# Kernel optimization log

Hardware: AMD Instinct MI355X
Metric: run time of the kernel (lower is better)

## Reference

```python
import jax, jax.numpy as jnp
import numpy as np

N = 16384   # total gate nodes (64 graphs x 256 gates)
B = 64      # graphs in batch
E = 49152   # directed edges (avg in-degree 3)
Q = 32      # qubit_num
F = 256     # feat_dim
D = 2 * F   # node feature dim = 512
H = 2       # heads
A = 128     # action_num


def _gatv2(x, wl, wr, att, b, src, dst, n):
    # PyG GATv2Conv (concat=True, share_weights=False, negative_slope=0.2)
    h, c = att.shape
    xl = (x @ wl).reshape(n, h, c)   # source-side projection [N,H,C]
    xr = (x @ wr).reshape(n, h, c)   # target-side projection [N,H,C]
    e = jax.nn.leaky_relu(xl[src] + xr[dst], 0.2)       # [E,H,C]
    logit = jnp.einsum('ehc,hc->eh', e, att)             # [E,H]
    m = jax.ops.segment_max(logit, dst, num_segments=n)  # softmax over in-edges per target
    p = jnp.exp(logit - m[dst])
    den = jax.ops.segment_sum(p, dst, num_segments=n)
    alpha = p / den[dst]                                 # [E,H]
    out = jax.ops.segment_sum(alpha[:, :, None] * xl[src], dst, num_segments=n)
    return out.reshape(n, h * c) + b


def _forward(x, xt_w1, xt_b1, xt_w2, xt_b2,
             g0_wl, g0_wr, g0_att, g0_b,
             g1_wl, g1_wr, g1_att, g1_b,
             g2_wl, g2_wr, g2_att, g2_b,
             g3_wl, g3_wr, g3_att, g3_b,
             g4_wl, g4_wr, g4_att, g4_b,
             ln_w, ln_b, aggr_t,
             m_w1, m_b1, m_w2, m_b2, m_w3, m_b3,
             edge_index, batch):
    lr = lambda v: jax.nn.leaky_relu(v, 0.01)
    # x_trans: Linear -> LeakyReLU -> Linear, then fold qubit-pairs into one node
    h0 = lr(x @ xt_w1 + xt_b1) @ xt_w2 + xt_b2           # [2N, F]
    cx = h0.reshape(-1, D)                               # [N, 2F]
    n = cx.shape[0]
    # GATv2Conv default add_self_loops=True (inputs contain no self loops)
    sl = jnp.arange(n, dtype=edge_index.dtype)
    src = jnp.concatenate([edge_index[0], sl])
    dst = jnp.concatenate([edge_index[1], sl])
    res = cx
    h = lr(_gatv2(cx, g0_wl, g0_wr, g0_att, g0_b, src, dst, n))
    for wl_, wr_, att_, b_ in ((g1_wl, g1_wr, g1_att, g1_b),
                               (g2_wl, g2_wr, g2_att, g2_b),
                               (g3_wl, g3_wr, g3_att, g3_b)):
        h = lr(_gatv2(h, wl_, wr_, att_, b_, src, dst, n))
    h = lr(_gatv2(h, g4_wl, g4_wr, g4_att, g4_b, src, dst, n))
    h = h + res                                           # residual [N, 2F]
    # PyG LayerNorm(mode='graph'): normalize over nodes AND channels per graph
    cnt = jax.ops.segment_sum(jnp.ones((n,), h.dtype), batch, num_segments=B)
    norm = cnt * h.shape[1]
    mean = jax.ops.segment_sum(h.sum(-1), batch, num_segments=B) / norm
    hc = h - mean[batch][:, None]
    var = jax.ops.segment_sum((hc * hc).sum(-1), batch, num_segments=B) / norm
    h = hc / jnp.sqrt(var + 1e-5)[batch][:, None] * ln_w + ln_b
    # SoftmaxAggregation(learn=True): channel-wise softmax over nodes per graph
    logit = h * aggr_t
    mg = jax.ops.segment_max(logit, batch, num_segments=B)
    p = jnp.exp(logit - mg[batch])
    den = jax.ops.segment_sum(p, batch, num_segments=B)
    g = jax.ops.segment_sum((p / den[batch]) * h, batch, num_segments=B)  # [B, 2F]
    # head MLP 512->384->256->128
    o = lr(g @ m_w1 + m_b1)
    o = lr(o @ m_w2 + m_b2)
    return o @ m_w3 + m_b3


def setup_inputs() -> dict:
    key = jax.random.key(0)
    ks = iter(jax.random.split(key, 64))
    def rn(shp, s=0.05):
        return jax.random.normal(next(ks), shp, jnp.float32) * s
    d = {}
    d['x'] = jax.random.normal(next(ks), (2 * N, Q), jnp.float32)
    src = jax.random.randint(next(ks), (E,), 0, N, jnp.int32)
    off = jax.random.randint(next(ks), (E,), 1, N, jnp.int32)
    d['edge_index'] = jnp.stack([src, (src + off) % N])  # no self loops
    d['batch'] = jnp.arange(N, dtype=jnp.int32) // (N // B)
    d['xt_w1'] = rn((Q, F)); d['xt_b1'] = rn((F,))
    d['xt_w2'] = rn((F, F)); d['xt_b2'] = rn((F,))
    d['g0_wl'] = rn((D, H * D)); d['g0_wr'] = rn((D, H * D))
    d['g0_att'] = rn((H, D));    d['g0_b'] = rn((H * D,))
    for i in (1, 2, 3):
        d[f'g{i}_wl'] = rn((H * D, H * D)); d[f'g{i}_wr'] = rn((H * D, H * D))
        d[f'g{i}_att'] = rn((H, D));        d[f'g{i}_b'] = rn((H * D,))
    d['g4_wl'] = rn((H * D, D)); d['g4_wr'] = rn((H * D, D))
    d['g4_att'] = rn((1, D));    d['g4_b'] = rn((D,))
    d['ln_w'] = jnp.ones((D,), jnp.float32); d['ln_b'] = jnp.zeros((D,), jnp.float32)
    d['aggr_t'] = jnp.array(1.0, jnp.float32)
    d['m_w1'] = rn((D, 384)); d['m_b1'] = rn((384,))
    d['m_w2'] = rn((384, 256)); d['m_b2'] = rn((256,))
    d['m_w3'] = rn((256, A)); d['m_b3'] = rn((A,))
    return d


def reference(x, edge_index, batch, xt_w1, xt_b1, xt_w2, xt_b2,
              g0_wl, g0_wr, g0_att, g0_b,
              g1_wl, g1_wr, g1_att, g1_b,
              g2_wl, g2_wr, g2_att, g2_b,
              g3_wl, g3_wr, g3_att, g3_b,
              g4_wl, g4_wr, g4_att, g4_b,
              ln_w, ln_b, aggr_t,
              m_w1, m_b1, m_w2, m_b2, m_w3, m_b3):
    return _forward(x, xt_w1, xt_b1, xt_w2, xt_b2,
                    g0_wl, g0_wr, g0_att, g0_b,
                    g1_wl, g1_wr, g1_att, g1_b,
                    g2_wl, g2_wr, g2_att, g2_b,
                    g3_wl, g3_wr, g3_att, g3_b,
                    g4_wl, g4_wr, g4_att, g4_b,
                    ln_w, ln_b, aggr_t,
                    m_w1, m_b1, m_w2, m_b2, m_w3, m_b3,
                    edge_index, batch)
```

## Files before the change

kernel.cpp:

```cpp
#include <hip/hip_runtime.h>
#include <hip/hip_bf16.h>

typedef __hip_bfloat16 bf16;

#define NN 16384
#define BBG 64
#define EE 49152
#define ET (EE + NN)
#define DD 512
#define NG (NN / BBG)

__device__ __forceinline__ float b2f(bf16 v) { return __bfloat162float(v); }
__device__ __forceinline__ bf16 f2b(float v) { return __float2bfloat16(v); }
__device__ __forceinline__ float sb2f(short s) {
    unsigned u = ((unsigned)(unsigned short)s) << 16;
    return __builtin_bit_cast(float, u);
}
__device__ __forceinline__ short f2bs(float v) {
    bf16 b = f2b(v);
    return __builtin_bit_cast(short, b);
}
__device__ __forceinline__ int clampi(int v, int lo, int hi)
{
    return v < lo ? lo : (v > hi ? hi : v);
}

typedef __attribute__((ext_vector_type(8))) short bf16x8;
typedef __attribute__((ext_vector_type(4))) float f32x4;

#define AS1 __attribute__((address_space(1)))
#define AS3 __attribute__((address_space(3)))

__global__ __launch_bounds__(256) void gemm_mfma_bt(
    const bf16* __restrict__ A, const bf16* __restrict__ Bt,
    const float* __restrict__ bias, float* __restrict__ C,
    bf16* __restrict__ Cb, int M, int N, int K, float slope, int has_act)
{
    __shared__ bf16 As[128 * 32];
    __shared__ bf16 Bs[128 * 32];
    const int tid = threadIdx.x;
    const int w = tid >> 6;
    const int l = tid & 63;
    const int bm = blockIdx.y * 128;
    const int bn = blockIdx.x * 128;
    const int wrow = (w >> 1) * 64;
    const int wcol = (w & 1) * 64;
    const int quad = l >> 4;
    const int c16 = l & 15;

    const int lrow = l >> 2;
    const int lchunk = l & 3;
    const bf16* Ag = A + (size_t)(bm + w * 16 + lrow) * K + lchunk * 8;
    const bf16* Bg = Bt + (size_t)(bn + w * 16 + lrow) * K + lchunk * 8;
    char* AsB = (char*)As;
    char* BsB = (char*)Bs;

    f32x4 acc[4][4] = {};

    for (int k0 = 0; k0 < K; k0 += 32) {
        __builtin_amdgcn_global_load_lds((const AS1 void*)(Ag + k0),
            (AS3 void*)(AsB + w * 1024), 16, 0, 0);
        __builtin_amdgcn_global_load_lds((const AS1 void*)(Ag + (size_t)64 * K + k0),
            (AS3 void*)(AsB + 4096 + w * 1024), 16, 0, 0);
        __builtin_amdgcn_global_load_lds((const AS1 void*)(Bg + k0),
            (AS3 void*)(BsB + w * 1024), 16, 0, 0);
        __builtin_amdgcn_global_load_lds((const AS1 void*)(Bg + (size_t)64 * K + k0),
            (AS3 void*)(BsB + 4096 + w * 1024), 16, 0, 0);
        __syncthreads();

        bf16x8 a[4], b[4];
#pragma unroll
        for (int i = 0; i < 4; i++) {
            int ra = wrow + i * 16 + c16;
            a[i] = *(const bf16x8*)(AsB + ra * 64 + quad * 16);
            int rb = wcol + i * 16 + c16;
            b[i] = *(const bf16x8*)(BsB + rb * 64 + quad * 16);
        }
#pragma unroll
        for (int i = 0; i < 4; i++)
#pragma unroll
            for (int j = 0; j < 4; j++)
                acc[i][j] = __builtin_amdgcn_mfma_f32_16x16x32_bf16(
                    a[i], b[j], acc[i][j], 0, 0, 0);
        __syncthreads();
    }

#pragma unroll
    for (int i = 0; i < 4; i++) {
#pragma unroll
        for (int j = 0; j < 4; j++) {
            int col = bn + wcol + j * 16 + c16;
            float bv = bias ? bias[col] : 0.f;
#pragma unroll
            for (int r = 0; r < 4; r++) {
                int row = bm + wrow + i * 16 + quad * 4 + r;
                float v = acc[i][j][r] + bv;
                if (has_act) v = (v >= 0.f) ? v : v * slope;
                if (C)  C[(size_t)row * N + col] = v;
                if (Cb) Cb[(size_t)row * N + col] = f2b(v);
            }
        }
    }
}

__global__ __launch_bounds__(256) void gemm_mfma_dual(
    const bf16* __restrict__ A, const bf16* __restrict__ Bt,
    bf16* __restrict__ X0, bf16* __restrict__ X1,
    int M, int Ntot, int K, int HC)
{
    __shared__ bf16 As[128 * 32];
    __shared__ bf16 Bs[128 * 32];
    const int tid = threadIdx.x;
    const int w = tid >> 6;
    const int l = tid & 63;
    const int bm = blockIdx.y * 128;
    const int bn = blockIdx.x * 128;
    const int wrow = (w >> 1) * 64;
    const int wcol = (w & 1) * 64;
    const int quad = l >> 4;
    const int c16 = l & 15;

    const int lrow = l >> 2;
    const int lchunk = l & 3;
    const bf16* Ag = A + (size_t)(bm + w * 16 + lrow) * K + lchunk * 8;
    const bf16* Bg = Bt + (size_t)(bn + w * 16 + lrow) * K + lchunk * 8;
    char* AsB = (char*)As;
    char* BsB = (char*)Bs;

    f32x4 acc[4][4] = {};

    for (int k0 = 0; k0 < K; k0 += 32) {
        __builtin_amdgcn_global_load_lds((const AS1 void*)(Ag + k0),
            (AS3 void*)(AsB + w * 1024), 16, 0, 0);
        __builtin_amdgcn_global_load_lds((const AS1 void*)(Ag + (size_t)64 * K + k0),
            (AS3 void*)(AsB + 4096 + w * 1024), 16, 0, 0);
        __builtin_amdgcn_global_load_lds((const AS1 void*)(Bg + k0),
            (AS3 void*)(BsB + w * 1024), 16, 0, 0);
        __builtin_amdgcn_global_load_lds((const AS1 void*)(Bg + (size_t)64 * K + k0),
            (AS3 void*)(BsB + 4096 + w * 1024), 16, 0, 0);
        __syncthreads();

        bf16x8 a[4], b[4];
#pragma unroll
        for (int i = 0; i < 4; i++) {
            int ra = wrow + i * 16 + c16;
            a[i] = *(const bf16x8*)(AsB + ra * 64 + quad * 16);
            int rb = wcol + i * 16 + c16;
            b[i] = *(const bf16x8*)(BsB + rb * 64 + quad * 16);
        }
#pragma unroll
        for (int i = 0; i < 4; i++)
#pragma unroll
            for (int j = 0; j < 4; j++)
                acc[i][j] = __builtin_amdgcn_mfma_f32_16x16x32_bf16(
                    a[i], b[j], acc[i][j], 0, 0, 0);
        __syncthreads();
    }

#pragma unroll
    for (int i = 0; i < 4; i++) {
#pragma unroll
        for (int j = 0; j < 4; j++) {
            int col = bn + wcol + j * 16 + c16;
            bf16* dst = (col < HC) ? (X0 + col) : (X1 + col - HC);
#pragma unroll
            for (int r = 0; r < 4; r++) {
                int row = bm + wrow + i * 16 + quad * 4 + r;
                dst[(size_t)row * HC] = f2b(acc[i][j][r]);
            }
        }
    }
}

__global__ __launch_bounds__(256) void gemm_f32(
    const float* __restrict__ A, const float* __restrict__ W,
    const float* __restrict__ bias, float* __restrict__ C,
    int M, int N, int K, float slope, int has_act)
{
    const int BK = 16;
    __shared__ float Asm[BK][64 + 1];
    __shared__ float Wsm[BK][64 + 1];
    int tid = threadIdx.x;
    int bm = blockIdx.y * 64;
    int bn = blockIdx.x * 64;
    int tr = tid >> 4;
    int tc = tid & 15;
    float acc[4][4] = {};

    for (int k0 = 0; k0 < K; k0 += BK) {
        {
            int col = tid & 15;
            int row = tid >> 4;
#pragma unroll
            for (int p = 0; p < 4; p++) {
                int r = row + p * 16;
                Asm[col][r] = A[(size_t)(bm + r) * K + k0 + col];
            }
        }
        {
            int wc = tid & 63;
            int wr = tid >> 6;
#pragma unroll
            for (int p = 0; p < 4; p++) {
                int r = wr + p * 4;
                Wsm[r][wc] = W[(size_t)(k0 + r) * N + bn + wc];
            }
        }
        __syncthreads();
#pragma unroll
        for (int kk = 0; kk < BK; kk++) {
            float a[4], w[4];
#pragma unroll
            for (int i = 0; i < 4; i++) a[i] = Asm[kk][tr * 4 + i];
#pragma unroll
            for (int j = 0; j < 4; j++) w[j] = Wsm[kk][tc * 4 + j];
#pragma unroll
            for (int i = 0; i < 4; i++)
#pragma unroll
                for (int j = 0; j < 4; j++)
                    acc[i][j] += a[i] * w[j];
        }
        __syncthreads();
    }
#pragma unroll
    for (int i = 0; i < 4; i++) {
        int r = bm + tr * 4 + i;
#pragma unroll
        for (int j = 0; j < 4; j++) {
            int cn = bn + tc * 4 + j;
            float v = acc[i][j];
            if (bias) v += bias[cn];
            if (has_act) v = (v >= 0.f) ? v : v * slope;
            C[(size_t)r * N + cn] = v;
        }
    }
}

__global__ __launch_bounds__(256) void transpose_f2b2(
    const float* __restrict__ in0, bf16* __restrict__ out0,
    const float* __restrict__ in1, bf16* __restrict__ out1, int R, int C)
{
    const float* in = blockIdx.z ? in1 : in0;
    bf16* out = blockIdx.z ? out1 : out0;
    __shared__ float tile[32][33];
    int c0 = blockIdx.x * 32;
    int r0 = blockIdx.y * 32;
    int tx = threadIdx.x & 31;
    int ty = threadIdx.x >> 5;
#pragma unroll
    for (int k = 0; k < 4; k++) {
        int r = ty + k * 8;
        tile[r][tx] = in[(size_t)(r0 + r) * C + c0 + tx];
    }
    __syncthreads();
#pragma unroll
    for (int k = 0; k < 4; k++) {
        int rr = ty + k * 8;
        out[(size_t)(c0 + rr) * R + r0 + tx] = f2b(tile[tx][rr]);
    }
}

__global__ void f2b_vec(const float* __restrict__ in, bf16* __restrict__ out, int n)
{
    int i = blockIdx.x * 256 + threadIdx.x;
    if (i < n) out[i] = f2b(in[i]);
}

__global__ void count_deg(const int* __restrict__ ei, int* __restrict__ deg)
{
    int e = blockIdx.x * 256 + threadIdx.x;
    if (e >= ET) return;
    int d = (e < EE) ? ei[EE + e] : (e - EE);
    d = clampi(d, 0, NN - 1);
    atomicAdd(&deg[d], 1);
}

__global__ __launch_bounds__(256) void scan_deg(const int* __restrict__ deg,
                                                int* __restrict__ rs)
{
    __shared__ int part[256];
    __shared__ int psum[257];
    int tid = threadIdx.x;
    const int per = NN / 256;
    int base = tid * per;
    int s = 0;
    for (int i = 0; i < per; i++) s += deg[base + i];
    part[tid] = s;
    __syncthreads();
    if (tid == 0) {
        int acc = 0;
        for (int i = 0; i < 256; i++) { psum[i] = acc; acc += part[i]; }
        psum[256] = acc;
    }
    __syncthreads();
    int acc = psum[tid];
    for (int i = 0; i < per; i++) { rs[base + i] = acc; acc += deg[base + i]; }
    if (tid == 0) rs[NN] = psum[256];
}

__global__ void fill_csr(const int* __restrict__ ei, const int* __restrict__ rs,
                         int* __restrict__ cur, int* __restrict__ csrc)
{
    int e = blockIdx.x * 256 + threadIdx.x;
    if (e >= ET) return;
    int s, d;
    if (e < EE) { s = ei[e]; d = ei[EE + e]; } else { s = d = e - EE; }
    s = clampi(s, 0, NN - 1);
    d = clampi(d, 0, NN - 1);
    int pos = atomicAdd(&cur[d], 1);
    int slot = clampi(rs[d] + pos, 0, ET - 1);
    csrc[slot] = s;
}

template<int HC, int PF>
__global__ __launch_bounds__(256, 4) void gat_wave3(
    const bf16* __restrict__ xl, const bf16* __restrict__ xr,
    const float* __restrict__ att, const float* __restrict__ bias,
    const int* __restrict__ rs, const int* __restrict__ csrc,
    const float* __restrict__ res, float* __restrict__ out_f,
    bf16* __restrict__ out_b, float* __restrict__ lnsums)
{
    constexpr int CPL = HC / 64;
    constexpr int NV = CPL / 8;
    const int tid = threadIdx.x;
    const int w = tid >> 6;
    const int lane = tid & 63;
    const int n = blockIdx.x * 4 + w;
    const int c0 = lane * CPL;

    int start = rs[n];
    int deg = clampi(rs[n + 1] - start, 1, 64);
    start = clampi(start, 0, ET - 1);
    start = __builtin_amdgcn_readfirstlane(start);
    deg = __builtin_amdgcn_readfirstlane(deg);
    int my_src = 0;
    if (lane < deg) my_src = clampi(csrc[start + lane], 0, NN - 1);

    bf16x8 rp[NV];
#pragma unroll
    for (int v = 0; v < NV; v++)
        rp[v] = *(const bf16x8*)(xr + (size_t)n * HC + c0 + v * 8);
    float av[CPL];
#pragma unroll
    for (int k = 0; k < CPL; k++) av[k] = att[c0 + k];

    bf16x8 rows[PF][NV];
#pragma unroll
    for (int r = 0; r < PF; r++) {
        if (r < deg) {
            int s = __shfl(my_src, r);
            const bf16* rpp = xl + (size_t)s * HC + c0;
#pragma unroll
            for (int v = 0; v < NV; v++) rows[r][v] = *(const bf16x8*)(rpp + v * 8);
        }
    }
    __builtin_amdgcn_sched_barrier(0);

    float rv[CPL];
#pragma unroll
    for (int k = 0; k < CPL; k++) rv[k] = sb2f(rp[k / 8][k % 8]);

    float part[PF];
#pragma unroll
    for (int r = 0; r < PF; r++) part[r] = -1e30f;
#pragma unroll
    for (int r = 0; r < PF; r++) {
        if (r < deg) {
            float p0 = 0.f, p1 = 0.f, p2 = 0.f, p3 = 0.f;
#pragma unroll
            for (int k = 0; k < CPL; k += 4) {
                float x0 = sb2f(rows[r][(k + 0) / 8][(k + 0) % 8]);
                float x1 = sb2f(rows[r][(k + 1) / 8][(k + 1) % 8]);
                float x2 = sb2f(rows[r][(k + 2) / 8][(k + 2) % 8]);
                float x3 = sb2f(rows[r][(k + 3) / 8][(k + 3) % 8]);
                float u0 = x0 + rv[k + 0]; u0 = (u0 >= 0.f) ? u0 : 0.2f * u0;
                float u1 = x1 + rv[k + 1]; u1 = (u1 >= 0.f) ? u1 : 0.2f * u1;
                float u2 = x2 + rv[k + 2]; u2 = (u2 >= 0.f) ? u2 : 0.2f * u2;
                float u3 = x3 + rv[k + 3]; u3 = (u3 >= 0.f) ? u3 : 0.2f * u3;
                p0 = fmaf(av[k + 0], u0, p0);
                p1 = fmaf(av[k + 1], u1, p1);
                p2 = fmaf(av[k + 2], u2, p2);
                p3 = fmaf(av[k + 3], u3, p3);
            }
            part[r] = (p0 + p1) + (p2 + p3);
        }
    }

    constexpr int MSK0 = (HC == 1024) ? 16 : 32;
#pragma unroll
    for (int msk = MSK0; msk; msk >>= 1) {
#pragma unroll
        for (int r = 0; r < PF; r++)
            if (r < deg) part[r] += __shfl_xor(part[r], msk);
    }

    float m = part[0];
#pragma unroll
    for (int r = 1; r < PF; r++)
        if (r < deg) m = fmaxf(m, part[r]);
    float den = 0.f;
    float pw[PF];
#pragma unroll
    for (int r = 0; r < PF; r++) {
        pw[r] = 0.f;
        if (r < deg) { pw[r] = __expf(part[r] - m); den += pw[r]; }
    }

    float acc[CPL];
#pragma unroll
    for (int k = 0; k < CPL; k++) acc[k] = 0.f;
#pragma unroll
    for (int r = 0; r < PF; r++) {
        if (r < deg) {
#pragma unroll
            for (int k = 0; k < CPL; k++)
                acc[k] = fmaf(pw[r], sb2f(rows[r][k / 8][k % 8]), acc[k]);
        }
    }

    if (deg > PF) {
        auto process = [&](bf16x8 (&rw)[NV]) {
            float part_t = 0.f;
#pragma unroll
            for (int k = 0; k < CPL; k++) {
                float x = sb2f(rw[k / 8][k % 8]);
                float u = x + rv[k];
                u = (u >= 0.f) ? u : 0.2f * u;
                part_t = fmaf(av[k], u, part_t);
            }
#pragma unroll
            for (int msk = MSK0; msk; msk >>= 1) part_t += __shfl_xor(part_t, msk);
            float lg = part_t;
            float mn = fmaxf(m, lg);
            float rr = __expf(m - mn);
            float pi = __expf(lg - mn);
            m = mn;
            den = den * rr + pi;
#pragma unroll
            for (int k = 0; k < CPL; k++) {
                float x = sb2f(rw[k / 8][k % 8]);
                acc[k] = fmaf(acc[k], rr, pi * x);
            }
        };
        bf16x8 curv[NV], nxt[NV];
        {
            int s = __shfl(my_src, PF);
            const bf16* rpp = xl + (size_t)s * HC + c0;
#pragma unroll
            for (int v = 0; v < NV; v++) curv[v] = *(const bf16x8*)(rpp + v * 8);
        }
        for (int i = PF; i < deg; i++) {
            if (i + 1 < deg) {
                int s = __shfl(my_src, i + 1);
                const bf16* rpp = xl + (size_t)s * HC + c0;
#pragma unroll
                for (int v = 0; v < NV; v++) nxt[v] = *(const bf16x8*)(rpp + v * 8);
            }
            process(curv);
#pragma unroll
            for (int v = 0; v < NV; v++) curv[v] = nxt[v];
        }
    }

    float inv = 1.f / den;
    float ls = 0.f, ls2 = 0.f;
    float vals[CPL];
#pragma unroll
    for (int k = 0; k < CPL; k++) {
        float v = fmaf(acc[k], inv, bias[c0 + k]);
        v = (v >= 0.f) ? v : 0.01f * v;
        vals[k] = v;
    }
    if (res) {
#pragma unroll
        for (int k = 0; k < CPL; k++) {
            vals[k] += res[(size_t)n * HC + c0 + k];
            ls += vals[k];
            ls2 += vals[k] * vals[k];
        }
#pragma unroll
        for (int v = 0; v < NV * 2; v++) {
            f32x4 ov;
#pragma unroll
            for (int k = 0; k < 4; k++) ov[k] = vals[v * 4 + k];
            *(f32x4*)(out_f + (size_t)n * HC + c0 + v * 4) = ov;
        }
    } else {
#pragma unroll
        for (int v = 0; v < NV; v++) {
            bf16x8 ov;
#pragma unroll
            for (int k = 0; k < 8; k++) ov[k] = f2bs(vals[v * 8 + k]);
            *(bf16x8*)(out_b + (size_t)n * HC + c0 + v * 8) = ov;
        }
    }

    if (lnsums) {
#pragma unroll
        for (int msk = 32; msk; msk >>= 1) {
            ls += __shfl_xor(ls, msk);
            ls2 += __shfl_xor(ls2, msk);
        }
        if (lane == 0) {
            int g = n >> 8;
            atomicAdd(&lnsums[g], ls);
            atomicAdd(&lnsums[BBG + g], ls2);
        }
    }
}

__global__ __launch_bounds__(256) void aggr_partial(
    const float* __restrict__ h, const float* __restrict__ lnsums,
    const float* __restrict__ lnw, const float* __restrict__ lnb,
    const float* __restrict__ t_, float* __restrict__ pm,
    float* __restrict__ pd, float* __restrict__ pa)
{
    int g = blockIdx.x, ch = blockIdx.y, nk = blockIdx.z;
    int tid = threadIdx.x;
    int c = ch * 256 + tid;
    const float tot = (float)(NG * DD);
    float S = lnsums[g], S2 = lnsums[BBG + g];
    float mu = S / tot;
    float iv = rsqrtf(fmaxf(S2 / tot - mu * mu, 0.f) + 1e-5f);
    float w = lnw[c], b = lnb[c], t = t_[0];
    size_t base = (size_t)g * NG * DD + (size_t)nk * 32 * DD + c;
    float m = -1e30f, den = 0.f, acc = 0.f;
    for (int i = 0; i < 32; i++) {
        float hn = (h[base + (size_t)i * DD] - mu) * iv * w + b;
        float lg = hn * t;
        if (lg > m) {
            float r = __expf(m - lg);
            den *= r; acc *= r; m = lg;
        }
        float p = __expf(lg - m);
        den += p; acc += p * hn;
    }
    size_t idx = (((size_t)g * 2 + ch) * 8 + nk) * 256 + tid;
    pm[idx] = m; pd[idx] = den; pa[idx] = acc;
}

__global__ __launch_bounds__(256) void aggr_combine(
    const float* __restrict__ pm, const float* __restrict__ pd,
    const float* __restrict__ pa, float* __restrict__ gout)
{
    int g = blockIdx.x, ch = blockIdx.y;
    int tid = threadIdx.x;
    size_t base = (((size_t)g * 2 + ch) * 8) * 256 + tid;
    float m = -1e30f;
#pragma unroll
    for (int k = 0; k < 8; k++) m = fmaxf(m, pm[base + k * 256]);
    float den = 0.f, acc = 0.f;
#pragma unroll
    for (int k = 0; k < 8; k++) {
        float r = __expf(pm[base + k * 256] - m);
        den += pd[base + k * 256] * r;
        acc += pa[base + k * 256] * r;
    }
    gout[(size_t)g * DD + ch * 256 + tid] = acc / den;
}

extern "C" void kernel_launch(void* const* d_in, const int* in_sizes, int n_in,
                              void* d_out, int out_size, void* d_ws, size_t ws_size,
                              hipStream_t stream)
{
    const float* x      = (const float*)d_in[0];
    const int*   ei     = (const int*)d_in[1];
    const float* xt_w1  = (const float*)d_in[3];
    const float* xt_b1  = (const float*)d_in[4];
    const float* xt_w2  = (const float*)d_in[5];
    const float* xt_b2  = (const float*)d_in[6];
    const float* ln_w   = (const float*)d_in[27];
    const float* ln_b   = (const float*)d_in[28];
    const float* aggr_t = (const float*)d_in[29];
    const float* m_w1   = (const float*)d_in[30];
    const float* m_b1   = (const float*)d_in[31];
    const float* m_w2   = (const float*)d_in[32];
    const float* m_b2   = (const float*)d_in[33];
    const float* m_w3   = (const float*)d_in[34];
    const float* m_b3   = (const float*)d_in[35];
    float* out = (float*)d_out;

    char* p = (char*)d_ws;
    auto take = [&](size_t bytes) {
        char* r = p;
        p += (bytes + 255) & ~(size_t)255;
        return r;
    };
    int* i_deg     = (int*)take((size_t)(NN + 1) * 4);
    int* i_rs      = (int*)take((size_t)(NN + 1) * 4);
    int* i_cur     = (int*)take((size_t)NN * 4);
    int* i_src     = (int*)take((size_t)ET * 4);
    float* f_sums  = (float*)take((size_t)2 * BBG * 4);
    float* f_pm    = (float*)take((size_t)BBG * 2 * 8 * 256 * 4);
    float* f_pd    = (float*)take((size_t)BBG * 2 * 8 * 256 * 4);
    float* f_pa    = (float*)take((size_t)BBG * 2 * 8 * 256 * 4);
    float* b_g     = (float*)take((size_t)BBG * DD * 4);
    float* b_m1    = (float*)take((size_t)BBG * 384 * 4);
    float* b_m2    = (float*)take((size_t)BBG * 256 * 4);
    float* b_res   = (float*)take((size_t)NN * DD * 4);
    float* b_h     = (float*)take((size_t)NN * DD * 4);
    bf16* b_resb   = (bf16*)take((size_t)NN * DD * 2);
    bf16* b_hb     = (bf16*)take((size_t)NN * 1024 * 2);
    bf16* b_xlb    = (bf16*)take((size_t)NN * 1024 * 2);
    bf16* b_xrb    = (bf16*)take((size_t)NN * 1024 * 2);
    bf16* b_xb     = (bf16*)take((size_t)2 * NN * 32 * 2);
    bf16* b_wcat   = (bf16*)take((size_t)2048 * 1024 * 2);
    bf16* b_w1b    = (bf16*)take((size_t)32 * 256 * 2);
    bf16* b_w2b    = (bf16*)take((size_t)256 * 256 * 2);
    bf16* b_t1b = b_hb;

    dim3 blk(256);

    hipMemsetAsync(i_deg, 0, (size_t)(NN + 1) * 4, stream);
    hipMemsetAsync(i_cur, 0, (size_t)NN * 4, stream);
    hipMemsetAsync(f_sums, 0, (size_t)2 * BBG * 4, stream);
    count_deg<<<ET / 256, blk, 0, stream>>>(ei, i_deg);
    scan_deg<<<1, blk, 0, stream>>>(i_deg, i_rs);
    fill_csr<<<ET / 256, blk, 0, stream>>>(ei, i_rs, i_cur, i_src);

    f2b_vec<<<(2 * NN * 32 + 255) / 256, blk, 0, stream>>>(x, b_xb, 2 * NN * 32);
    transpose_f2b2<<<dim3(256 / 32, 32 / 32, 1), blk, 0, stream>>>(
        xt_w1, b_w1b, xt_w1, b_w1b, 32, 256);
    transpose_f2b2<<<dim3(256 / 32, 256 / 32, 1), blk, 0, stream>>>(
        xt_w2, b_w2b, xt_w2, b_w2b, 256, 256);

    gemm_mfma_bt<<<dim3(256 / 128, 32768 / 128), blk, 0, stream>>>(
        b_xb, b_w1b, xt_b1, (float*)nullptr, b_t1b, 32768, 256, 32, 0.01f, 1);
    gemm_mfma_bt<<<dim3(256 / 128, 32768 / 128), blk, 0, stream>>>(
        b_t1b, b_w2b, xt_b2, b_res, b_resb, 32768, 256, 256, 0.f, 0);

    for (int L = 0; L < 5; L++) {
        const float* wl  = (const float*)d_in[7 + 4 * L];
        const float* wr  = (const float*)d_in[8 + 4 * L];
        const float* att = (const float*)d_in[9 + 4 * L];
        const float* gb  = (const float*)d_in[10 + 4 * L];
        int Fin = (L == 0) ? 512 : 1024;
        int HC  = (L == 4) ? 512 : 1024;
        const bf16* hin = (L == 0) ? b_resb : b_hb;

        transpose_f2b2<<<dim3(HC / 32, Fin / 32, 2), blk, 0, stream>>>(
            wl, b_wcat, wr, b_wcat + (size_t)HC * Fin, Fin, HC);
        gemm_mfma_dual<<<dim3(2 * HC / 128, NN / 128), blk, 0, stream>>>(
            hin, b_wcat, b_xlb, b_xrb, NN, 2 * HC, Fin, HC);
        if (L == 4) {
            gat_wave3<512, 8><<<NN / 4, blk, 0, stream>>>(
                b_xlb, b_xrb, att, gb, i_rs, i_src,
                b_res, b_h, (bf16*)nullptr, f_sums);
        } else {
            gat_wave3<1024, 6><<<NN / 4, blk, 0, stream>>>(
                b_xlb, b_xrb, att, gb, i_rs, i_src,
                (const float*)nullptr, (float*)nullptr, b_hb, (float*)nullptr);
        }
    }

    aggr_partial<<<dim3(BBG, 2, 8), blk, 0, stream>>>(
        b_h, f_sums, ln_w, ln_b, aggr_t, f_pm, f_pd, f_pa);
    aggr_combine<<<dim3(BBG, 2), blk, 0, stream>>>(f_pm, f_pd, f_pa, b_g);

    gemm_f32<<<dim3(384 / 64, 1), blk, 0, stream>>>(
        b_g, m_w1, m_b1, b_m1, 64, 384, 512, 0.01f, 1);
    gemm_f32<<<dim3(256 / 64, 1), blk, 0, stream>>>(
        b_m1, m_w2, m_b2, b_m2, 64, 256, 384, 0.01f, 1);
    gemm_f32<<<dim3(128 / 64, 1), blk, 0, stream>>>(
        b_m2, m_w3, m_b3, out, 64, 128, 256, 0.f, 0);
}
```

Measured before the change: 1.179 ms.

## Split GATv2 attention per head across wavefronts with branchless prefetch of neighbor rows

The GAT aggregation kernel now assigns one wavefront per (node, head) pair for the two-head layers, so each lane handles 8 channels instead of 16, and the grid doubles. The first 8 neighbor rows are loaded unconditionally by clamping indices to the last valid neighbor, and masking happens only in the softmax weights. An asm barrier keeps the loads grouped ahead of compute. The aim is more parallelism and memory-level concurrency with fewer registers, at the cost of redundant xr/att/index loads per head. The tail loop loses its software prefetch.

```diff
diff --git a/kernel.cpp b/kernel.cpp
--- a/kernel.cpp
+++ b/kernel.cpp
@@ -312,187 +312,169 @@
     csrc[slot] = s;
 }
 
-template<int HC, int PF>
-__global__ __launch_bounds__(256, 4) void gat_wave3(
+template<int NH>
+__global__ __launch_bounds__(256, 4) void gat_wave4(
     const bf16* __restrict__ xl, const bf16* __restrict__ xr,
     const float* __restrict__ att, const float* __restrict__ bias,
     const int* __restrict__ rs, const int* __restrict__ csrc,
     const float* __restrict__ res, float* __restrict__ out_f,
     bf16* __restrict__ out_b, float* __restrict__ lnsums)
 {
-    constexpr int CPL = HC / 64;
-    constexpr int NV = CPL / 8;
+    constexpr int HC = NH * 512;
+    constexpr int PF = 8;
     const int tid = threadIdx.x;
     const int w = tid >> 6;
     const int lane = tid & 63;
-    const int n = blockIdx.x * 4 + w;
-    const int c0 = lane * CPL;
+    const int gw = blockIdx.x * 4 + w;
+    const int n  = (NH == 2) ? (gw >> 1) : gw;
+    const int h  = (NH == 2) ? (gw & 1) : 0;
+    const int cb = h * 512 + lane * 8;
 
     int start = rs[n];
     int deg = clampi(rs[n + 1] - start, 1, 64);
     start = clampi(start, 0, ET - 1);
     start = __builtin_amdgcn_readfirstlane(start);
     deg = __builtin_amdgcn_readfirstlane(deg);
-    int my_src = 0;
-    if (lane < deg) my_src = clampi(csrc[start + lane], 0, NN - 1);
-
-    bf16x8 rp[NV];
-#pragma unroll
-    for (int v = 0; v < NV; v++)
-        rp[v] = *(const bf16x8*)(xr + (size_t)n * HC + c0 + v * 8);
-    float av[CPL];
-#pragma unroll
-    for (int k = 0; k < CPL; k++) av[k] = att[c0 + k];
-
-    bf16x8 rows[PF][NV];
+    const int dm1 = deg - 1;
+    int my_src = csrc[start + ((lane < deg) ? lane : dm1)];
+    my_src = clampi(my_src, 0, NN - 1);
+
+    f32x4 rpx = *(const f32x4*)(xr + (size_t)n * HC + cb);
+    f32x4 a0 = *(const f32x4*)(att + cb);
+    f32x4 a1 = *(const f32x4*)(att + cb + 4);
+    f32x4 rows[PF];
 #pragma unroll
     for (int r = 0; r < PF; r++) {
-        if (r < deg) {
-            int s = __shfl(my_src, r);
-            const bf16* rpp = xl + (size_t)s * HC + c0;
-#pragma unroll
-            for (int v = 0; v < NV; v++) rows[r][v] = *(const bf16x8*)(rpp + v * 8);
-        }
-    }
-    __builtin_amdgcn_sched_barrier(0);
-
-    float rv[CPL];
-#pragma unroll
-    for (int k = 0; k < CPL; k++) rv[k] = sb2f(rp[k / 8][k % 8]);
+        int s = __shfl(my_src, (r < dm1) ? r : dm1);
+        rows[r] = *(const f32x4*)(xl + (size_t)s * HC + cb);
+    }
+    asm volatile("" : "+v"(rpx), "+v"(rows[0]), "+v"(rows[1]), "+v"(rows[2]),
+                      "+v"(rows[3]), "+v"(rows[4]), "+v"(rows[5]),
+                      "+v"(rows[6]), "+v"(rows[7]));
+
+    float rv[8], av[8];
+    {
+        bf16x8 xb = __builtin_bit_cast(bf16x8, rpx);
+#pragma unroll
+        for (int k = 0; k < 8; k++) rv[k] = sb2f(xb[k]);
+#pragma unroll
+        for (int k = 0; k < 4; k++) { av[k] = a0[k]; av[4 + k] = a1[k]; }
+    }
 
     float part[PF];
 #pragma unroll
-    for (int r = 0; r < PF; r++) part[r] = -1e30f;
-#pragma unroll
     for (int r = 0; r < PF; r++) {
-        if (r < deg) {
-            float p0 = 0.f, p1 = 0.f, p2 = 0.f, p3 = 0.f;
-#pragma unroll
-            for (int k = 0; k < CPL; k += 4) {
-                float x0 = sb2f(rows[r][(k + 0) / 8][(k + 0) % 8]);
-                float x1 = sb2f(rows[r][(k + 1) / 8][(k + 1) % 8]);
-                float x2 = sb2f(rows[r][(k + 2) / 8][(k + 2) % 8]);
-                float x3 = sb2f(rows[r][(k + 3) / 8][(k + 3) % 8]);
-                float u0 = x0 + rv[k + 0]; u0 = (u0 >= 0.f) ? u0 : 0.2f * u0;
-                float u1 = x1 + rv[k + 1]; u1 = (u1 >= 0.f) ? u1 : 0.2f * u1;
-                float u2 = x2 + rv[k + 2]; u2 = (u2 >= 0.f) ? u2 : 0.2f * u2;
-                float u3 = x3 + rv[k + 3]; u3 = (u3 >= 0.f) ? u3 : 0.2f * u3;
-                p0 = fmaf(av[k + 0], u0, p0);
-                p1 = fmaf(av[k + 1], u1, p1);
-                p2 = fmaf(av[k + 2], u2, p2);
-                p3 = fmaf(av[k + 3], u3, p3);
-            }
-            part[r] = (p0 + p1) + (p2 + p3);
-        }
-    }
-
-    constexpr int MSK0 = (HC == 1024) ? 16 : 32;
-#pragma unroll
-    for (int msk = MSK0; msk; msk >>= 1) {
-#pragma unroll
-        for (int r = 0; r < PF; r++)
-            if (r < deg) part[r] += __shfl_xor(part[r], msk);
-    }
-
-    float m = part[0];
-#pragma unroll
-    for (int r = 1; r < PF; r++)
-        if (r < deg) m = fmaxf(m, part[r]);
+        bf16x8 rb = __builtin_bit_cast(bf16x8, rows[r]);
+        float p0 = 0.f, p1 = 0.f, p2 = 0.f, p3 = 0.f;
+#pragma unroll
+        for (int k = 0; k < 8; k += 4) {
+            float x0 = sb2f(rb[k + 0]);
+            float x1 = sb2f(rb[k + 1]);
+            float x2 = sb2f(rb[k + 2]);
+            float x3 = sb2f(rb[k + 3]);
+            float u0 = x0 + rv[k + 0]; u0 = (u0 >= 0.f) ? u0 : 0.2f * u0;
+            float u1 = x1 + rv[k + 1]; u1 = (u1 >= 0.f) ? u1 : 0.2f * u1;
+            float u2 = x2 + rv[k + 2]; u2 = (u2 >= 0.f) ? u2 : 0.2f * u2;
+            float u3 = x3 + rv[k + 3]; u3 = (u3 >= 0.f) ? u3 : 0.2f * u3;
+            p0 = fmaf(av[k + 0], u0, p0);
+            p1 = fmaf(av[k + 1], u1, p1);
+            p2 = fmaf(av[k + 2], u2, p2);
+            p3 = fmaf(av[k + 3], u3, p3);
+        }
+        part[r] = (p0 + p1) + (p2 + p3);
+    }
+
+#pragma unroll
+    for (int msk = 32; msk; msk >>= 1) {
+#pragma unroll
+        for (int r = 0; r < PF; r++) part[r] += __shfl_xor(part[r], msk);
+    }
+
+    float m = -1e30f;
+#pragma unroll
+    for (int r = 0; r < PF; r++) {
+        float vr = (r < deg) ? part[r] : -1e30f;
+        m = fmaxf(m, vr);
+    }
     float den = 0.f;
     float pw[PF];
 #pragma unroll
     for (int r = 0; r < PF; r++) {
-        pw[r] = 0.f;
-        if (r < deg) { pw[r] = __expf(part[r] - m); den += pw[r]; }
-    }
-
-    float acc[CPL];
-#pragma unroll
-    for (int k = 0; k < CPL; k++) acc[k] = 0.f;
+        float e = __expf(part[r] - m);
+        pw[r] = (r < deg) ? e : 0.f;
+        den += pw[r];
+    }
+
+    float acc[8];
+#pragma unroll
+    for (int k = 0; k < 8; k++) acc[k] = 0.f;
 #pragma unroll
     for (int r = 0; r < PF; r++) {
-        if (r < deg) {
-#pragma unroll
-            for (int k = 0; k < CPL; k++)
-                acc[k] = fmaf(pw[r], sb2f(rows[r][k / 8][k % 8]), acc[k]);
-        }
+        bf16x8 rb = __builtin_bit_cast(bf16x8, rows[r]);
+#pragma unroll
+        for (int k = 0; k < 8; k++)
+            acc[k] = fmaf(pw[r], sb2f(rb[k]), acc[k]);
     }
 
     if (deg > PF) {
-        auto process = [&](bf16x8 (&rw)[NV]) {
-            float part_t = 0.f;
-#pragma unroll
-            for (int k = 0; k < CPL; k++) {
-                float x = sb2f(rw[k / 8][k % 8]);
+        for (int i = PF; i < deg; i++) {
+            int s = __shfl(my_src, i);
+            f32x4 rw = *(const f32x4*)(xl + (size_t)s * HC + cb);
+            bf16x8 rb = __builtin_bit_cast(bf16x8, rw);
+            float pt = 0.f;
+#pragma unroll
+            for (int k = 0; k < 8; k++) {
+                float x = sb2f(rb[k]);
                 float u = x + rv[k];
                 u = (u >= 0.f) ? u : 0.2f * u;
-                part_t = fmaf(av[k], u, part_t);
+                pt = fmaf(av[k], u, pt);
             }
 #pragma unroll
-            for (int msk = MSK0; msk; msk >>= 1) part_t += __shfl_xor(part_t, msk);
-            float lg = part_t;
-            float mn = fmaxf(m, lg);
+            for (int msk = 32; msk; msk >>= 1) pt += __shfl_xor(pt, msk);
+            float mn = fmaxf(m, pt);
             float rr = __expf(m - mn);
-            float pi = __expf(lg - mn);
+            float pi = __expf(pt - mn);
             m = mn;
             den = den * rr + pi;
 #pragma unroll
-            for (int k = 0; k < CPL; k++) {
-                float x = sb2f(rw[k / 8][k % 8]);
+            for (int k = 0; k < 8; k++) {
+                float x = sb2f(rb[k]);
                 acc[k] = fmaf(acc[k], rr, pi * x);
             }
-        };
-        bf16x8 curv[NV], nxt[NV];
-        {
-            int s = __shfl(my_src, PF);
-            const bf16* rpp = xl + (size_t)s * HC + c0;
-#pragma unroll
-            for (int v = 0; v < NV; v++) curv[v] = *(const bf16x8*)(rpp + v * 8);
-        }
-        for (int i = PF; i < deg; i++) {
-            if (i + 1 < deg) {
-                int s = __shfl(my_src, i + 1);
-                const bf16* rpp = xl + (size_t)s * HC + c0;
-#pragma unroll
-                for (int v = 0; v < NV; v++) nxt[v] = *(const bf16x8*)(rpp + v * 8);
-            }
-            process(curv);
-#pragma unroll
-            for (int v = 0; v < NV; v++) curv[v] = nxt[v];
         }
     }
 
     float inv = 1.f / den;
+    f32x4 b0 = *(const f32x4*)(bias + cb);
+    f32x4 b1 = *(const f32x4*)(bias + cb + 4);
     float ls = 0.f, ls2 = 0.f;
-    float vals[CPL];
-#pragma unroll
-    for (int k = 0; k < CPL; k++) {
-        float v = fmaf(acc[k], inv, bias[c0 + k]);
+    float vals[8];
+#pragma unroll
+    for (int k = 0; k < 8; k++) {
+        float bv = (k < 4) ? b0[k] : b1[k - 4];
+        float v = fmaf(acc[k], inv, bv);
         v = (v >= 0.f) ? v : 0.01f * v;
         vals[k] = v;
     }
     if (res) {
 #pragma unroll
-        for (int k = 0; k < CPL; k++) {
-            vals[k] += res[(size_t)n * HC + c0 + k];
+        for (int k = 0; k < 8; k++) {
+            vals[k] += res[(size_t)n * HC + cb + k];
             ls += vals[k];
             ls2 += vals[k] * vals[k];
         }
 #pragma unroll
-        for (int v = 0; v < NV * 2; v++) {
+        for (int v = 0; v < 2; v++) {
             f32x4 ov;
 #pragma unroll
             for (int k = 0; k < 4; k++) ov[k] = vals[v * 4 + k];
-            *(f32x4*)(out_f + (size_t)n * HC + c0 + v * 4) = ov;
+            *(f32x4*)(out_f + (size_t)n * HC + cb + v * 4) = ov;
         }
     } else {
-#pragma unroll
-        for (int v = 0; v < NV; v++) {
-            bf16x8 ov;
-#pragma unroll
-            for (int k = 0; k < 8; k++) ov[k] = f2bs(vals[v * 8 + k]);
-            *(bf16x8*)(out_b + (size_t)n * HC + c0 + v * 8) = ov;
-        }
+        bf16x8 ov;
+#pragma unroll
+        for (int k = 0; k < 8; k++) ov[k] = f2bs(vals[k]);
+        *(bf16x8*)(out_b + (size_t)n * HC + cb) = ov;
     }
 
     if (lnsums) {
@@ -643,11 +625,11 @@
         gemm_mfma_dual<<<dim3(2 * HC / 128, NN / 128), blk, 0, stream>>>(
             hin, b_wcat, b_xlb, b_xrb, NN, 2 * HC, Fin, HC);
         if (L == 4) {
-            gat_wave3<512, 8><<<NN / 4, blk, 0, stream>>>(
+            gat_wave4<1><<<NN / 4, blk, 0, stream>>>(
                 b_xlb, b_xrb, att, gb, i_rs, i_src,
                 b_res, b_h, (bf16*)nullptr, f_sums);
         } else {
-            gat_wave3<1024, 6><<<NN / 4, blk, 0, stream>>>(
+            gat_wave4<2><<<NN * 2 / 4, blk, 0, stream>>>(
                 b_xlb, b_xrb, att, gb, i_rs, i_src,
                 (const float*)nullptr, (float*)nullptr, b_hb, (float*)nullptr);
         }
```

Result: faster. 1.091 ms (-7.5%).
